# Optimization experiments

Measured on AMD Instinct MI355X. Metric: run time of the kernel, lower is better.

Reference implementation:

```python
import jax, jax.numpy as jnp
import numpy as np

IMAGE = 128            # canvas_size == image_size -> resize is identity
N_LINES = 32
N_SEGMENTS = 2
N_POINTS = 5           # control points per line (2 shared-endpoint quadratic beziers)
N_COLOR = 3
COORDPAIRS = np.array([[0, 1, 2], [2, 3, 4]])  # (n_segments, 3)
N_SAMPLES = 10         # polyline samples for bezier edt2 (explicit 10 in source)
POWER = 2.0            # power at progress=0 (= config.power_i)
SIGMA2 = 0.05          # annealed sigma2 at progress=0
EPS = 1e-10
BS = 4


def setup_inputs() -> dict:
    key = jax.random.key(0)
    k1, k2, k3, k4 = jax.random.split(key, 4)
    position = 0.5 * jax.random.normal(k1, (BS, N_LINES, N_POINTS * 2), jnp.float32)
    radius = jax.random.uniform(k2, (BS, N_LINES, 1), jnp.float32, minval=0.3, maxval=1.0)
    color = jax.random.uniform(k3, (BS, N_LINES, N_COLOR), jnp.float32)
    background = jax.random.uniform(k4, (BS, N_COLOR), jnp.float32)
    return {"position": position, "radius": radius, "color": color, "background": background}


def _render(position, radius, color, background):
    bs = position.shape[0]
    r = jnp.linspace(-1.0, 1.0, IMAGE)
    gy, gx = jnp.meshgrid(r, r, indexing="ij")
    grid = jnp.stack([gy, gx], axis=-1)                      # (H, W, 2)

    # --- reshape_params (background='keep', n_back=0) ---
    lines = position.reshape(bs, N_LINES, N_POINTS, 2)
    segs = lines[:, :, COORDPAIRS]                           # (bs, nl, nseg, 3, 2)
    # smooth bezier: reflect control point of segments after the first
    segs = segs.at[:, :, 1:, 1].set(2.0 * segs[:, :, 1:, 0] - segs[:, :, 1:, 1])
    curves = segs.reshape(bs, N_LINES * N_SEGMENTS, 3, 2)    # (bs, N, 3, 2)

    sigma = (radius ** 2).reshape(bs, N_LINES, 1, 1)
    sigma = jnp.repeat(sigma, N_SEGMENTS, axis=1) * SIGMA2   # (bs, N, 1, 1)
    col = jnp.repeat(color, N_SEGMENTS, axis=1)[:, :, :, None, None]  # (bs, N, nc, 1, 1)

    # --- curve_edt2_polyline: sample quadratic bezier, min segment distance ---
    t = jnp.linspace(0.0, 1.0, N_SAMPLES)
    w = jnp.stack([(1.0 - t) ** 2, 2.0 * t * (1.0 - t), t ** 2], axis=0)  # (3, T)
    pts = jnp.einsum("bnkc,kt->bntc", curves, w)             # (bs, N, T, 2)
    a, b = pts[:, :, :-1], pts[:, :, 1:]                     # (bs, N, S=T-1, 2)
    v = b - a
    v_ = v[:, :, :, None, None, :]
    d = grid[None, None, None] - a[:, :, :, None, None, :]   # (bs, N, S, H, W, 2)
    vv = jnp.sum(v * v, axis=-1)[:, :, :, None, None]
    tp = jnp.clip(jnp.sum(d * v_, axis=-1) / (vv + EPS), 0.0, 1.0)
    diff = d - tp[..., None] * v_
    edt2 = jnp.min(jnp.sum(diff * diff, axis=-1), axis=2)    # (bs, N, H, W)

    # --- intensity + rasterize + over-composite ---
    intensity = jnp.exp(-((edt2 / sigma) ** POWER))          # (bs, N, H, W)
    rasters = col * intensity[:, :, None]                    # (bs, N, nc, H, W)
    canvas = jnp.broadcast_to(background[:, None, :, None, None],
                              (bs, 1, N_COLOR, IMAGE, IMAGE))
    rasters = jnp.concatenate([rasters, canvas], axis=1)     # (bs, N+1, nc, H, W)
    inten_c = jnp.broadcast_to(intensity[:, :, None],
                               (bs, intensity.shape[1], N_COLOR, IMAGE, IMAGE))
    inten_all = jnp.concatenate([inten_c, jnp.ones_like(canvas)], axis=1)
    linv = 1.0 - inten_all + EPS
    # 'over' composite front-to-back along stroke dim: exclusive cumprod weights
    w_excl = jnp.concatenate([jnp.ones_like(linv[:, :1]),
                              jnp.cumprod(linv, axis=1)[:, :-1]], axis=1)
    images = jnp.sum(rasters * w_excl, axis=1)               # (bs, nc, H, W)
    return jnp.clip(images, 0.0, 1.0)


def reference(position, radius, color, background):
    return _render(position, radius, color, background)
```

## Files before the change

kernel.cpp:

```cpp
#include <hip/hip_runtime.h>

#define IMAGE   128
#define NLINES  32
#define NCURVE  64
#define NSUB    9
#define PIX     (IMAGE*IMAGE)
#define BS      4
#define NCHUNK  8
#define CPC     8

__global__ __launch_bounds__(512, 8)
void render_kernel(const float* __restrict__ pos,
                   const float* __restrict__ rad,
                   const float* __restrict__ col,
                   const float* __restrict__ bg,
                   float* __restrict__ out)
{
    __shared__ float4 s_sub4[NCURVE*NSUB];
    __shared__ float2 s_sub2[NCURVE*NSUB];
    __shared__ float4 s_cur[NCURVE];
    __shared__ float4 s_part[NCHUNK*64];

    const int tid  = threadIdx.x;
    const int b    = blockIdx.x >> 8;
    const int tile = blockIdx.x & 255;

    for (int e = tid; e < NCURVE*NSUB; e += 512) {
        const int n    = e / NSUB;
        const int j    = e - n*NSUB;
        const int line = n >> 1;
        const int seg  = n & 1;
        const float* P = pos + (b*NLINES + line)*10;
        float c0x, c0y, c1x, c1y, c2x, c2y;
        if (seg == 0) {
            c0x = P[0]; c0y = P[1];
            c1x = P[2]; c1y = P[3];
            c2x = P[4]; c2y = P[5];
        } else {
            const float q2x = P[4], q2y = P[5];
            const float q3x = P[6], q3y = P[7];
            c0x = q2x;             c0y = q2y;
            c1x = 2.0f*q2x - q3x;  c1y = 2.0f*q2y - q3y;
            c2x = P[8];            c2y = P[9];
        }
        const float t0 = (float)j     * (1.0f/9.0f);
        const float t1 = (float)(j+1) * (1.0f/9.0f);
        float ax, ay, bx, by;
        {
            const float mt = 1.0f - t0;
            const float w0 = mt*mt, w1 = 2.0f*t0*mt, w2 = t0*t0;
            ax = w0*c0x + w1*c1x + w2*c2x;
            ay = w0*c0y + w1*c1y + w2*c2y;
        }
        {
            const float mt = 1.0f - t1;
            const float w0 = mt*mt, w1 = 2.0f*t1*mt, w2 = t1*t1;
            bx = w0*c0x + w1*c1x + w2*c2x;
            by = w0*c0y + w1*c1y + w2*c2y;
        }
        const float vx = bx - ax, vy = by - ay;
        const float rvv = 1.0f / (vx*vx + vy*vy + 1e-10f);
        s_sub4[e] = make_float4(ax, ay, vx, vy);
        s_sub2[e] = make_float2(vx*rvv, vy*rvv);
    }
    if (tid < NCURVE) {
        const int line = tid >> 1;
        const float r  = rad[b*NLINES + line];
        s_cur[tid] = make_float4(1.0f / (r*r*0.05f),
                                 col[(b*NLINES + line)*3 + 0],
                                 col[(b*NLINES + line)*3 + 1],
                                 col[(b*NLINES + line)*3 + 2]);
    }
    __syncthreads();

    const int px    = tid & 63;
    const int chunk = tid >> 6;
    const int p     = tile*64 + px;
    const float g0  = -1.0f + (float)(p >> 7)  * (2.0f/127.0f);
    const float g1  = -1.0f + (float)(p & 127) * (2.0f/127.0f);

    float aR = 0.0f, aG = 0.0f, aB = 0.0f, T = 1.0f;
    for (int i = 0; i < CPC; ++i) {
        const int n = chunk*CPC + i;
        float edt2 = 3.4e38f;
        #pragma unroll 3
        for (int j = 0; j < NSUB; ++j) {
            const float4 s = s_sub4[n*NSUB + j];
            const float2 w = s_sub2[n*NSUB + j];
            const float d0 = g0 - s.x;
            const float d1 = g1 - s.y;
            const float tp = fminf(fmaxf(d0*w.x + d1*w.y, 0.0f), 1.0f);
            const float e0 = fmaf(-tp, s.z, d0);
            const float e1 = fmaf(-tp, s.w, d1);
            edt2 = fminf(edt2, fmaf(e0, e0, e1*e1));
        }
        const float4 cu = s_cur[n];
        const float xs  = edt2 * cu.x;
        const float I   = __expf(-xs*xs);
        const float wI  = I * T;
        aR = fmaf(cu.y, wI, aR);
        aG = fmaf(cu.z, wI, aG);
        aB = fmaf(cu.w, wI, aB);
        T *= (1.0f - I + 1e-10f);
    }
    s_part[chunk*64 + px] = make_float4(aR, aG, aB, T);
    __syncthreads();

    if (tid < 64) {
        float4 acc = s_part[tid];
        float C0 = acc.x, C1 = acc.y, C2 = acc.z, Tt = acc.w;
        #pragma unroll
        for (int c = 1; c < NCHUNK; ++c) {
            const float4 q = s_part[c*64 + tid];
            C0 = fmaf(Tt, q.x, C0);
            C1 = fmaf(Tt, q.y, C1);
            C2 = fmaf(Tt, q.z, C2);
            Tt *= q.w;
        }
        C0 = fmaf(Tt, bg[b*3+0], C0);
        C1 = fmaf(Tt, bg[b*3+1], C1);
        C2 = fmaf(Tt, bg[b*3+2], C2);
        const int po = tile*64 + tid;
        out[(b*3+0)*PIX + po] = fminf(fmaxf(C0, 0.0f), 1.0f);
        out[(b*3+1)*PIX + po] = fminf(fmaxf(C1, 0.0f), 1.0f);
        out[(b*3+2)*PIX + po] = fminf(fmaxf(C2, 0.0f), 1.0f);
    }
}

extern "C" void kernel_launch(void* const* d_in, const int* in_sizes, int n_in,
                              void* d_out, int out_size, void* d_ws, size_t ws_size,
                              hipStream_t stream) {
    const float* pos = (const float*)d_in[0];
    const float* rad = (const float*)d_in[1];
    const float* col = (const float*)d_in[2];
    const float* bg  = (const float*)d_in[3];
    float* out = (float*)d_out;

    render_kernel<<<dim3(BS*256), dim3(512), 0, stream>>>(pos, rad, col, bg, out);
}
```

Measured before the change: 70.08 us.

## Process four pixels per thread to amortize segment setup and LDS loads

Each thread now evaluates four pixels, reusing every shared-memory segment load across them, and the grid shrinks fourfold so per-block bezier sampling setup is done once per 256 pixels instead of 64. Launch bounds are relaxed to allow more registers for the per-pixel arrays. The trade-off is one block per CU and fewer waves to hide latency, relying on the added instruction-level parallelism instead.

```diff
diff --git a/kernel.cpp b/kernel.cpp
--- a/kernel.cpp
+++ b/kernel.cpp
@@ -8,8 +8,9 @@
 #define BS      4
 #define NCHUNK  8
 #define CPC     8
+#define PPL     4
 
-__global__ __launch_bounds__(512, 8)
+__global__ __launch_bounds__(512, 2)
 void render_kernel(const float* __restrict__ pos,
                    const float* __restrict__ rad,
                    const float* __restrict__ col,
@@ -19,11 +20,11 @@
     __shared__ float4 s_sub4[NCURVE*NSUB];
     __shared__ float2 s_sub2[NCURVE*NSUB];
     __shared__ float4 s_cur[NCURVE];
-    __shared__ float4 s_part[NCHUNK*64];
+    __shared__ float4 s_part[NCHUNK*256];
 
     const int tid  = threadIdx.x;
-    const int b    = blockIdx.x >> 8;
-    const int tile = blockIdx.x & 255;
+    const int b    = blockIdx.x >> 6;
+    const int tile = blockIdx.x & 63;
 
     for (int e = tid; e < NCURVE*NSUB; e += 512) {
         const int n    = e / NSUB;
@@ -73,45 +74,61 @@
     }
     __syncthreads();
 
-    const int px    = tid & 63;
+    const int lane  = tid & 63;
     const int chunk = tid >> 6;
-    const int p     = tile*64 + px;
-    const float g0  = -1.0f + (float)(p >> 7)  * (2.0f/127.0f);
-    const float g1  = -1.0f + (float)(p & 127) * (2.0f/127.0f);
 
-    float aR = 0.0f, aG = 0.0f, aB = 0.0f, T = 1.0f;
+    float g0[PPL], g1[PPL];
+    float aR[PPL], aG[PPL], aB[PPL], T[PPL];
+    #pragma unroll
+    for (int k = 0; k < PPL; ++k) {
+        const int p = tile*256 + k*64 + lane;
+        g0[k] = -1.0f + (float)(p >> 7)  * (2.0f/127.0f);
+        g1[k] = -1.0f + (float)(p & 127) * (2.0f/127.0f);
+        aR[k] = 0.0f; aG[k] = 0.0f; aB[k] = 0.0f; T[k] = 1.0f;
+    }
+
     for (int i = 0; i < CPC; ++i) {
         const int n = chunk*CPC + i;
-        float edt2 = 3.4e38f;
+        float edt2[PPL];
+        #pragma unroll
+        for (int k = 0; k < PPL; ++k) edt2[k] = 3.4e38f;
         #pragma unroll 3
         for (int j = 0; j < NSUB; ++j) {
             const float4 s = s_sub4[n*NSUB + j];
             const float2 w = s_sub2[n*NSUB + j];
-            const float d0 = g0 - s.x;
-            const float d1 = g1 - s.y;
-            const float tp = fminf(fmaxf(d0*w.x + d1*w.y, 0.0f), 1.0f);
-            const float e0 = fmaf(-tp, s.z, d0);
-            const float e1 = fmaf(-tp, s.w, d1);
-            edt2 = fminf(edt2, fmaf(e0, e0, e1*e1));
+            #pragma unroll
+            for (int k = 0; k < PPL; ++k) {
+                const float d0 = g0[k] - s.x;
+                const float d1 = g1[k] - s.y;
+                const float tp = fminf(fmaxf(d0*w.x + d1*w.y, 0.0f), 1.0f);
+                const float e0 = fmaf(-tp, s.z, d0);
+                const float e1 = fmaf(-tp, s.w, d1);
+                edt2[k] = fminf(edt2[k], fmaf(e0, e0, e1*e1));
+            }
         }
         const float4 cu = s_cur[n];
-        const float xs  = edt2 * cu.x;
-        const float I   = __expf(-xs*xs);
-        const float wI  = I * T;
-        aR = fmaf(cu.y, wI, aR);
-        aG = fmaf(cu.z, wI, aG);
-        aB = fmaf(cu.w, wI, aB);
-        T *= (1.0f - I + 1e-10f);
+        #pragma unroll
+        for (int k = 0; k < PPL; ++k) {
+            const float xs = edt2[k] * cu.x;
+            const float I  = __expf(-xs*xs);
+            const float wI = I * T[k];
+            aR[k] = fmaf(cu.y, wI, aR[k]);
+            aG[k] = fmaf(cu.z, wI, aG[k]);
+            aB[k] = fmaf(cu.w, wI, aB[k]);
+            T[k] *= (1.0f - I + 1e-10f);
+        }
     }
-    s_part[chunk*64 + px] = make_float4(aR, aG, aB, T);
+    #pragma unroll
+    for (int k = 0; k < PPL; ++k)
+        s_part[chunk*256 + k*64 + lane] = make_float4(aR[k], aG[k], aB[k], T[k]);
     __syncthreads();
 
-    if (tid < 64) {
+    if (tid < 256) {
         float4 acc = s_part[tid];
         float C0 = acc.x, C1 = acc.y, C2 = acc.z, Tt = acc.w;
         #pragma unroll
         for (int c = 1; c < NCHUNK; ++c) {
-            const float4 q = s_part[c*64 + tid];
+            const float4 q = s_part[c*256 + tid];
             C0 = fmaf(Tt, q.x, C0);
             C1 = fmaf(Tt, q.y, C1);
             C2 = fmaf(Tt, q.z, C2);
@@ -120,7 +137,7 @@
         C0 = fmaf(Tt, bg[b*3+0], C0);
         C1 = fmaf(Tt, bg[b*3+1], C1);
         C2 = fmaf(Tt, bg[b*3+2], C2);
-        const int po = tile*64 + tid;
+        const int po = tile*256 + tid;
         out[(b*3+0)*PIX + po] = fminf(fmaxf(C0, 0.0f), 1.0f);
         out[(b*3+1)*PIX + po] = fminf(fmaxf(C1, 0.0f), 1.0f);
         out[(b*3+2)*PIX + po] = fminf(fmaxf(C2, 0.0f), 1.0f);
@@ -136,5 +153,5 @@
     const float* bg  = (const float*)d_in[3];
     float* out = (float*)d_out;
 
-    render_kernel<<<dim3(BS*256), dim3(512), 0, stream>>>(pos, rad, col, bg, out);
+    render_kernel<<<dim3(BS*64), dim3(512), 0, stream>>>(pos, rad, col, bg, out);
 }
```

Result: no change. 68.95 us (-1.6%).
